# Performance work log

Hardware: AMD Instinct MI355X
Metric: run time of the kernel (lower is better)

Reference implementation:

```python
import jax, jax.numpy as jnp
import numpy as np

B, L, D, OUT, EXP = 4, 4096, 128, 55, 2
D2 = 2 * D

def _ln(x, g, b):
    m = jnp.mean(x, axis=-1, keepdims=True)
    v = jnp.mean((x - m) ** 2, axis=-1, keepdims=True)
    return (x - m) / jnp.sqrt(v + 1e-5) * g + b

def setup_inputs() -> dict:
    key = jax.random.key(0)
    ks = iter(jax.random.split(key, 32))
    w = lambda shape: jax.random.normal(next(ks), shape, jnp.float32) * 0.02
    inp = {
        'x1': jax.random.normal(next(ks), (B, L, D), jnp.float32),
        'x2': jax.random.normal(next(ks), (B, L, D), jnp.float32),
        'ln1_g': jnp.ones((D,)), 'ln1_b': jnp.zeros((D,)),
        'ln2_g': jnp.ones((D,)), 'ln2_b': jnp.zeros((D,)),
        'Wq': w((D, D)), 'bq': jnp.zeros((D,)),
        'Wv1': w((D, D)), 'bv1': jnp.zeros((D,)),
        'Wk': w((D, D)), 'bk': jnp.zeros((D,)),
        'Wv2': w((D, D)), 'bv2': jnp.zeros((D,)),
        'Wp1': w((D, D)), 'bp1': jnp.zeros((D,)),
        'Wp2': w((D, D)), 'bp2': jnp.zeros((D,)),
        'lnf_g': jnp.ones((D2,)), 'lnf_b': jnp.zeros((D2,)),
        'Wf1': w((D2, EXP * D2)), 'bf1': jnp.zeros((EXP * D2,)),
        'Wf2': w((EXP * D2, D2)), 'bf2': jnp.zeros((D2,)),
        'ln3_g': jnp.ones((D2,)), 'ln3_b': jnp.zeros((D2,)),
        'Wo': w((D2, OUT)), 'bo': jnp.zeros((OUT,)),
    }
    return inp

def reference(x1, x2, ln1_g, ln1_b, ln2_g, ln2_b, Wq, bq, Wv1, bv1, Wk, bk,
              Wv2, bv2, Wp1, bp1, Wp2, bp2, lnf_g, lnf_b, Wf1, bf1, Wf2, bf2,
              ln3_g, ln3_b, Wo, bo):
    res1, res2 = x1, x2
    x1n = _ln(x1, ln1_g, ln1_b)
    x2n = _ln(x2, ln2_g, ln2_b)
    q1 = x1n @ Wq + bq        # [B,L,D]
    v1 = x1n @ Wv1 + bv1
    k2 = x2n @ Wk + bk
    v2 = x2n @ Wv2 + bv2
    # faithful to torch: energy = einsum('bqd,bkd->bqk', keys2, queries1)
    energy = jnp.einsum('bqd,bkd->bqk', k2, q1)
    att = jax.nn.softmax(energy / jnp.sqrt(jnp.float32(D)), axis=-1)  # [B,L,L]
    out1 = jnp.einsum('bal,blv->bav', att, v1) @ Wp1 + bp1
    out2 = jnp.einsum('bal,blv->bav', att, v2) @ Wp2 + bp2
    y1 = out1 + res1
    y2 = out2 + res2
    x = jnp.concatenate([y1, y2], axis=-1)  # [B,L,2D]
    res = x
    h = _ln(x, lnf_g, lnf_b)
    h = jax.nn.gelu(h @ Wf1 + bf1, approximate=False) @ Wf2 + bf2
    x = _ln(h + res, ln3_g, ln3_b)
    return x @ Wo + bo  # [B,L,OUT]
```

## Files before the change

kernel.cpp:

```cpp
#include <hip/hip_runtime.h>
#include <hip/hip_fp16.h>

typedef _Float16 half8 __attribute__((ext_vector_type(8)));
typedef float f32x4 __attribute__((ext_vector_type(4)));
typedef long lng2 __attribute__((ext_vector_type(2)));

#define B_   4
#define L_   4096
#define D_   128
#define M_   (B_*L_)
#define D2_  256
#define H_   512
#define OUT_ 55

__device__ __forceinline__ f32x4 mfma16(half8 a, half8 b, f32x4 c) {
    return __builtin_amdgcn_mfma_f32_16x16x32_f16(a, b, c, 0, 0, 0);
}
__device__ __forceinline__ f32x4 mfma8(long a, long b, f32x4 c) {
    return __builtin_amdgcn_mfma_f32_16x16x32_fp8_fp8(a, b, c, 0, 0, 0);
}
__device__ __forceinline__ int pk4(float a, float b, float c, float d) {
    int t = __builtin_amdgcn_cvt_pk_fp8_f32(a, b, 0, false);
    return __builtin_amdgcn_cvt_pk_fp8_f32(c, d, t, true);
}
__device__ __forceinline__ float fexp2(float x) { return __builtin_amdgcn_exp2f(x); }

#define KSCL (0.08838834764831845f * 1.4426950408889634f)

#define WQ_OFF   0
#define WV1_OFF  16384
#define WK_OFF   32768
#define WV2_OFF  49152
#define WP1_OFF  65536
#define WP2_OFF  81920
#define WF1_OFF  98304
#define WF2_OFF  229376
#define WO_OFF   360448


__global__ void prep_kernel(const float* Wq, const float* Wv1, const float* Wk,
                            const float* Wv2, const float* Wp1, const float* Wp2,
                            const float* Wf1, const float* Wf2, const float* Wo,
                            _Float16* wsw, float* rowsum) {
    int id = blockIdx.y;
    int t  = blockIdx.x * 256 + threadIdx.x;
    if (id == 9) {
        if (t < 4096) ((f32x4*)rowsum)[t] = f32x4{0.f, 0.f, 0.f, 0.f};
        return;
    }
    const float* src = nullptr; int K = 0, N = 0, Npad = 0, off = 0;
    switch (id) {
        case 0: src = Wq;  K = 128; N = 128; Npad = 128; off = WQ_OFF;  break;
        case 1: src = Wv1; K = 128; N = 128; Npad = 128; off = WV1_OFF; break;
        case 2: src = Wk;  K = 128; N = 128; Npad = 128; off = WK_OFF;  break;
        case 3: src = Wv2; K = 128; N = 128; Npad = 128; off = WV2_OFF; break;
        case 4: src = Wp1; K = 128; N = 128; Npad = 128; off = WP1_OFF; break;
        case 5: src = Wp2; K = 128; N = 128; Npad = 128; off = WP2_OFF; break;
        case 6: src = Wf1; K = 256; N = 512; Npad = 512; off = WF1_OFF; break;
        case 7: src = Wf2; K = 512; N = 256; Npad = 256; off = WF2_OFF; break;
        case 8: src = Wo;  K = 256; N = 55;  Npad = 64;  off = WO_OFF;  break;
        default: return;
    }
    int total = K * Npad;
    if (t >= total) return;
    int k = t / Npad, n = t % Npad;
    float v = (n < N) ? src[k * N + n] : 0.f;
    int s = k >> 5, c = n >> 4, ln = n & 15;
    int q, j;
    if (id == 4 || id == 5) { q = (k >> 2) & 3; j = (k & 3) + (((k >> 4) & 1) << 2); }
    else                    { q = (k >> 3) & 3; j = k & 7; }
    int nc = Npad >> 4;
    wsw[off + ((size_t)((s * nc + c) * 64 + q * 16 + ln)) * 8 + j] = (_Float16)v;
}


__global__ __launch_bounds__(256) void proj_kernel(const float* x1, const float* x2,
        const _Float16* wsw,
        const float* ln1_g, const float* ln1_b, const float* ln2_g, const float* ln2_b,
        const float* bq, const float* bv1, const float* bk, const float* bv2,
        _Float16* q1, _Float16* k2, unsigned char* vsw8) {
    int g2 = blockIdx.y;
    const float* X  = g2 ? x2 : x1;
    const float* lg = g2 ? ln2_g : ln1_g;
    const float* lb = g2 ? ln2_b : ln1_b;
    int wave = threadIdx.x >> 6, lane = threadIdx.x & 63;
    int quad = lane >> 4, ln = lane & 15;
    int mbase = blockIdx.x * 64 + wave * 16;
    int lt = mbase >> 4;

    const float* xr = X + (size_t)(mbase + ln) * D_;
    float xv[4][8];
    float sum = 0.f, sq = 0.f;
    #pragma unroll
    for (int s = 0; s < 4; s++) {
        f32x4 v0 = *(const f32x4*)(xr + s * 32 + quad * 8);
        f32x4 v1 = *(const f32x4*)(xr + s * 32 + quad * 8 + 4);
        #pragma unroll
        for (int j = 0; j < 4; j++) {
            xv[s][j]     = v0[j];
            xv[s][j + 4] = v1[j];
            sum += v0[j] + v1[j];
            sq  += v0[j] * v0[j] + v1[j] * v1[j];
        }
    }
    sum += __shfl_xor(sum, 16); sum += __shfl_xor(sum, 32);
    sq  += __shfl_xor(sq, 16);  sq  += __shfl_xor(sq, 32);
    float mean = sum * (1.f / 128.f);
    float var  = sq * (1.f / 128.f) - mean * mean;
    float inv  = rsqrtf(var + 1e-5f);
    half8 a[4];
    #pragma unroll
    for (int s = 0; s < 4; s++) {
        f32x4 g0 = *(const f32x4*)(lg + s * 32 + quad * 8);
        f32x4 g1 = *(const f32x4*)(lg + s * 32 + quad * 8 + 4);
        f32x4 b0 = *(const f32x4*)(lb + s * 32 + quad * 8);
        f32x4 b1 = *(const f32x4*)(lb + s * 32 + quad * 8 + 4);
        #pragma unroll
        for (int j = 0; j < 4; j++) {
            a[s][j]     = (_Float16)((xv[s][j] - mean) * inv * g0[j] + b0[j]);
            a[s][j + 4] = (_Float16)((xv[s][j + 4] - mean) * inv * g1[j] + b1[j]);
        }
    }

    {
        const _Float16* Bw = wsw + (g2 ? WK_OFF : WQ_OFF);
        const float* bias = g2 ? bk : bq;
        float scl = g2 ? KSCL : 1.f;
        _Float16* out = g2 ? k2 : q1;
        f32x4 acc[8];
        #pragma unroll
        for (int c = 0; c < 8; c++) acc[c] = f32x4{0.f, 0.f, 0.f, 0.f};
        half8 Wc[4], Wn[4];
        #pragma unroll
        for (int s = 0; s < 4; s++)
            Wc[s] = *(const half8*)(Bw + ((size_t)((s * 8 + 0) * 64 + lane)) * 8);
        #pragma unroll
        for (int c = 0; c < 8; c++) {
            int cn = (c < 7) ? c + 1 : 7;
            #pragma unroll
            for (int s = 0; s < 4; s++)
                Wn[s] = *(const half8*)(Bw + ((size_t)((s * 8 + cn) * 64 + lane)) * 8);
            #pragma unroll
            for (int s = 0; s < 4; s++)
                acc[c] = mfma16(a[s], Wc[s], acc[c]);
            #pragma unroll
            for (int s = 0; s < 4; s++) Wc[s] = Wn[s];
        }
        #pragma unroll
        for (int c = 0; c < 8; c++) {
            int n = c * 16 + ln;
            float bv = bias[n];
            #pragma unroll
            for (int r = 0; r < 4; r++) {
                int s_o = c >> 1, q_o = ((c & 1) << 1) | (ln >> 3), j = ln & 7;
                out[((size_t)((lt * 4 + s_o) * 64 + q_o * 16 + (quad * 4 + r))) * 8 + j]
                    = (_Float16)((acc[c][r] + bv) * scl);
            }
        }
    }

    {
        const _Float16* Bw = wsw + (g2 ? WV2_OFF : WV1_OFF);
        const float* bias = g2 ? bv2 : bv1;
        int cbase = g2 ? 8 : 0;
        f32x4 acc[8];
        #pragma unroll
        for (int c = 0; c < 8; c++) acc[c] = f32x4{0.f, 0.f, 0.f, 0.f};
        half8 Wc[4], Wn[4];
        #pragma unroll
        for (int s = 0; s < 4; s++)
            Wc[s] = *(const half8*)(Bw + ((size_t)((s * 8 + 0) * 64 + lane)) * 8);
        #pragma unroll
        for (int c = 0; c < 8; c++) {
            int cn = (c < 7) ? c + 1 : 7;
            #pragma unroll
            for (int s = 0; s < 4; s++)
                Wn[s] = *(const half8*)(Bw + ((size_t)((s * 8 + cn) * 64 + lane)) * 8);
            #pragma unroll
            for (int s = 0; s < 4; s++)
                acc[c] = mfma16(a[s], Wc[s], acc[c]);
            #pragma unroll
            for (int s = 0; s < 4; s++) Wc[s] = Wn[s];
        }
        int b = mbase >> 12;
        int l0 = (mbase & (L_ - 1)) + quad * 4;
        int sp = l0 >> 6, tt = (l0 >> 4) & 3, q2 = (l0 >> 2) & 3;
        unsigned char* Vb = vsw8 + (size_t)b * (1u << 20);
        #pragma unroll
        for (int c = 0; c < 8; c++) {
            int n = c * 16 + ln;
            float bv = bias[n];
            int pk = pk4(acc[c][0] + bv, acc[c][1] + bv, acc[c][2] + bv, acc[c][3] + bv);
            *(int*)(Vb + (((size_t)(sp * 16 + cbase + c) * 64 + q2 * 16 + ln) * 16 + tt * 4)) = pk;
        }
    }
}

__global__ __launch_bounds__(256) void score_kernel(
        const _Float16* __restrict__ q1sw, const _Float16* __restrict__ k2sw,
        unsigned char* __restrict__ pmat8, float* __restrict__ rowsum) {
    int w = threadIdx.x >> 6, lane = threadIdx.x & 63;
    int quad = lane >> 4, ln = lane & 15;
    int b = blockIdx.z;
    int kL0 = blockIdx.y * 128 + (w & 1) * 64;
    int mL0 = blockIdx.x * 128 + (w >> 1) * 64;
    int ltk = ((b << 12) + kL0) >> 4;
    int ltm = ((b << 12) + mL0) >> 4;

    f32x4 acc[4][4];
    #pragma unroll
    for (int i = 0; i < 4; i++)
        #pragma unroll
        for (int j = 0; j < 4; j++) acc[i][j] = f32x4{0.f, 0.f, 0.f, 0.f};

    #pragma unroll
    for (int s = 0; s < 4; s++) {
        half8 a[4], bq[4];
        #pragma unroll
        for (int i = 0; i < 4; i++)
            a[i] = *(const half8*)(q1sw + ((size_t)(((ltk + i) * 4 + s) * 64 + lane)) * 8);
        #pragma unroll
        for (int j = 0; j < 4; j++)
            bq[j] = *(const half8*)(k2sw + ((size_t)(((ltm + j) * 4 + s) * 64 + lane)) * 8);
        #pragma unroll
        for (int i = 0; i < 4; i++)
            #pragma unroll
            for (int j = 0; j < 4; j++)
                acc[i][j] = mfma16(a[i], bq[j], acc[i][j]);
    }

    unsigned char* Pb = pmat8 + (size_t)b * (16u << 20);
    int sp = kL0 >> 6;
    #pragma unroll
    for (int j = 0; j < 4; j++) {
        int4 d;
        float csum = 0.f;
        #pragma unroll
        for (int i = 0; i < 4; i++) {
            float p0 = fexp2(acc[i][j][0]);
            float p1 = fexp2(acc[i][j][1]);
            float p2 = fexp2(acc[i][j][2]);
            float p3 = fexp2(acc[i][j][3]);
            csum += (p0 + p1) + (p2 + p3);
            ((int*)&d)[i] = pk4(p0, p1, p2, p3);
        }
        csum += __shfl_xor(csum, 16);
        csum += __shfl_xor(csum, 32);
        if (lane < 16)
            atomicAdd(&rowsum[(b << 12) + mL0 + j * 16 + ln], csum);
        int lt = (mL0 >> 4) + j;
        *(int4*)(Pb + (((size_t)(lt * 64 + sp)) * 64 + lane) * 16) = d;
    }
}

__global__ __launch_bounds__(512) void pv_kernel(
        const unsigned char* __restrict__ pmat8, const unsigned char* __restrict__ vsw8,
        const float* __restrict__ rowsum,
        _Float16* __restrict__ att1, _Float16* __restrict__ att2) {
    __shared__ f32x4 part[4][2][4][64];
    int w = threadIdx.x >> 6, lane = threadIdx.x & 63;
    int quad = lane >> 4, ln = lane & 15;
    int wc = w & 3, kh = w >> 2;
    int rowG0 = blockIdx.x * 32;
    int b = rowG0 >> 12;
    int lt0 = (rowG0 & (L_ - 1)) >> 4;
    const unsigned char* Pb = pmat8 + (size_t)b * (16u << 20);
    const unsigned char* Vb = vsw8 + (size_t)b * (1u << 20);
    int c0 = wc * 4;
    int sp0 = kh * 32;

    f32x4 acc[4][2];
    #pragma unroll
    for (int i = 0; i < 4; i++)
        #pragma unroll
        for (int c = 0; c < 2; c++) acc[i][c] = f32x4{0.f, 0.f, 0.f, 0.f};

    lng2 Vf[2][4], Pf[2][2];
    #pragma unroll
    for (int p = 0; p < 2; p++) {
        #pragma unroll
        for (int i = 0; i < 4; i++)
            Vf[p][i] = *(const lng2*)(Vb + (((size_t)((sp0 + p) * 16 + c0 + i)) * 64 + lane) * 16);
        #pragma unroll
        for (int c = 0; c < 2; c++)
            Pf[p][c] = *(const lng2*)(Pb + (((size_t)((lt0 + c) * 64 + sp0 + p)) * 64 + lane) * 16);
    }

    #define PVSTEP(buf, ii) do {                                                     \
        int spn = sp0 + ((((ii) + 2) < 32) ? (ii) + 2 : 31);                         \
        lng2 Vn[4], Pn[2];                                                           \
        _Pragma("unroll")                                                            \
        for (int i = 0; i < 4; i++)                                                  \
            Vn[i] = *(const lng2*)(Vb + (((size_t)(spn * 16 + c0 + i)) * 64 + lane) * 16); \
        _Pragma("unroll")                                                            \
        for (int c = 0; c < 2; c++)                                                  \
            Pn[c] = *(const lng2*)(Pb + (((size_t)((lt0 + c) * 64 + spn)) * 64 + lane) * 16); \
        _Pragma("unroll")                                                            \
        for (int i = 0; i < 4; i++)                                                  \
            _Pragma("unroll")                                                        \
            for (int c = 0; c < 2; c++) {                                            \
                acc[i][c] = mfma8(Vf[buf][i].x, Pf[buf][c].x, acc[i][c]);             \
                acc[i][c] = mfma8(Vf[buf][i].y, Pf[buf][c].y, acc[i][c]);             \
            }                                                                        \
        _Pragma("unroll")                                                            \
        for (int i = 0; i < 4; i++) Vf[buf][i] = Vn[i];                              \
        _Pragma("unroll")                                                            \
        for (int c = 0; c < 2; c++) Pf[buf][c] = Pn[c];                              \
    } while (0)

    for (int ii = 0; ii < 32; ii += 2) {
        PVSTEP(0, ii);
        PVSTEP(1, ii + 1);
    }
    #undef PVSTEP

    if (kh == 1) {
        #pragma unroll
        for (int i = 0; i < 4; i++)
            #pragma unroll
            for (int c = 0; c < 2; c++)
                part[wc][c][i][lane] = acc[i][c];
    }
    __syncthreads();
    if (kh == 0) {
        #pragma unroll
        for (int i = 0; i < 4; i++)
            #pragma unroll
            for (int c = 0; c < 2; c++)
                acc[i][c] += part[wc][c][i][lane];

        _Float16* att = (wc >= 2) ? att2 : att1;
        #pragma unroll
        for (int c = 0; c < 2; c++) {
            float inv = 1.f / rowsum[rowG0 + c * 16 + ln];
            int lt = (rowG0 >> 4) + c;
            #pragma unroll
            for (int sl = 0; sl < 2; sl++) {
                half8 v;
                #pragma unroll
                for (int r = 0; r < 4; r++) {
                    v[r]     = (_Float16)(acc[2 * sl][c][r] * inv);
                    v[r + 4] = (_Float16)(acc[2 * sl + 1][c][r] * inv);
                }
                int s = (wc & 1) * 2 + sl;
                *(half8*)(att + ((size_t)((lt * 4 + s) * 64 + lane)) * 8) = v;
            }
        }
    }
}

__global__ __launch_bounds__(256) void attn_out_kernel(const _Float16* att1, const _Float16* att2,
        const _Float16* wsw, const float* bp1, const float* bp2,
        const float* x1, const float* x2, const float* lnf_g, const float* lnf_b,
        _Float16* res, _Float16* xn) {
    __shared__ float sst[2][16][2][2];
    int w = threadIdx.x >> 6, lane = threadIdx.x & 63;
    int quad = lane >> 4, ln = lane & 15;
    int rt = w & 1, st = w >> 1;
    int mbase = blockIdx.x * 32 + rt * 16;
    int lt = mbase >> 4;
    const _Float16* att = st ? att2 : att1;
    const _Float16* Wp = wsw + (st ? WP2_OFF : WP1_OFF);
    const float* bp = st ? bp2 : bp1;
    const float* xres = st ? x2 : x1;

    half8 a[4];
    #pragma unroll
    for (int s = 0; s < 4; s++)
        a[s] = *(const half8*)(att + ((size_t)((lt * 4 + s) * 64 + lane)) * 8);

    f32x4 y[8];
    #pragma unroll
    for (int c = 0; c < 8; c++) y[c] = f32x4{0,0,0,0};

    half8 Wc[4], Wn[4];
    #pragma unroll
    for (int s = 0; s < 4; s++)
        Wc[s] = *(const half8*)(Wp + ((size_t)((s * 8 + 0) * 64 + lane)) * 8);
    #pragma unroll
    for (int c = 0; c < 8; c++) {
        int cn = (c < 7) ? c + 1 : 7;
        #pragma unroll
        for (int s = 0; s < 4; s++)
            Wn[s] = *(const half8*)(Wp + ((size_t)((s * 8 + cn) * 64 + lane)) * 8);
        #pragma unroll
        for (int s = 0; s < 4; s++)
            y[c] = mfma16(a[s], Wc[s], y[c]);
        #pragma unroll
        for (int s = 0; s < 4; s++) Wc[s] = Wn[s];
    }

    float psum[4] = {0,0,0,0}, psq[4] = {0,0,0,0};
    #pragma unroll
    for (int c = 0; c < 8; c++) {
        int n = c * 16 + ln;
        float bv = bp[n];
        #pragma unroll
        for (int r = 0; r < 4; r++) {
            int m = mbase + quad * 4 + r;
            float v = y[c][r] + bv + xres[(size_t)m * D_ + n];
            y[c][r] = v; psum[r] += v; psq[r] += v * v;
        }
    }
    #pragma unroll
    for (int off = 1; off < 16; off <<= 1)
        #pragma unroll
        for (int r = 0; r < 4; r++) { psum[r] += __shfl_xor(psum[r], off); psq[r] += __shfl_xor(psq[r], off); }
    if (ln == 0)
        #pragma unroll
        for (int r = 0; r < 4; r++) {
            sst[rt][quad * 4 + r][st][0] = psum[r];
            sst[rt][quad * 4 + r][st][1] = psq[r];
        }
    __syncthreads();
    #pragma unroll
    for (int r = 0; r < 4; r++) {
        float su = sst[rt][quad * 4 + r][0][0] + sst[rt][quad * 4 + r][1][0];
        float sq = sst[rt][quad * 4 + r][0][1] + sst[rt][quad * 4 + r][1][1];
        float mean = su * (1.f / 256.f);
        float var = sq * (1.f / 256.f) - mean * mean;
        float inv = rsqrtf(var + 1e-5f);
        int m = mbase + quad * 4 + r;
        int lt_m = m >> 4;
        #pragma unroll
        for (int c = 0; c < 8; c++) {
            int colg = st * 128 + c * 16 + ln;
            res[(size_t)m * D2_ + colg] = (_Float16)y[c][r];
            float yn = (y[c][r] - mean) * inv * lnf_g[colg] + lnf_b[colg];
            int s_x = colg >> 5, q_x = (colg >> 3) & 3, j = colg & 7;
            xn[((size_t)((lt_m * 8 + s_x) * 64 + q_x * 16 + (m & 15))) * 8 + j] = (_Float16)yn;
        }
    }
}

__global__ __launch_bounds__(256) void ffn1_kernel(const _Float16* xn, const _Float16* wsw,
        const float* bf1, _Float16* h) {
    int wave = threadIdx.x >> 6, lane = threadIdx.x & 63;
    int quad = lane >> 4, ln = lane & 15;
    int mbase = blockIdx.x * 64 + wave * 16;
    int lt = mbase >> 4;
    int nt = blockIdx.y;
    const _Float16* W = wsw + WF1_OFF;

    half8 a[8];
    #pragma unroll
    for (int s = 0; s < 8; s++)
        a[s] = *(const half8*)(xn + ((size_t)((lt * 8 + s) * 64 + lane)) * 8);

    f32x4 acc[8];
    #pragma unroll
    for (int c = 0; c < 8; c++) acc[c] = f32x4{0,0,0,0};

    half8 Wc[8], Wn[8];
    #pragma unroll
    for (int s = 0; s < 8; s++)
        Wc[s] = *(const half8*)(W + ((size_t)((s * 32 + nt * 8) * 64 + lane)) * 8);
    #pragma unroll
    for (int c = 0; c < 8; c++) {
        int cn = (c < 7) ? c + 1 : 7;
        #pragma unroll
        for (int s = 0; s < 8; s++)
            Wn[s] = *(const half8*)(W + ((size_t)((s * 32 + nt * 8 + cn) * 64 + lane)) * 8);
        #pragma unroll
        for (int s = 0; s < 8; s++)
            acc[c] = mfma16(a[s], Wc[s], acc[c]);
        #pragma unroll
        for (int s = 0; s < 8; s++) Wc[s] = Wn[s];
    }
    #pragma unroll
    for (int c = 0; c < 8; c++) {
        int n = nt * 128 + c * 16 + ln;
        float bv = bf1[n];
        int s_h = n >> 5, q_h = (n >> 3) & 3, j = n & 7;
        #pragma unroll
        for (int r = 0; r < 4; r++) {
            float v = acc[c][r] + bv;
            float u = 0.7978845608f * (v + 0.044715f * v * v * v);
            float e = fexp2(-2.8853900818f * u);
            float ge = v * __builtin_amdgcn_rcpf(1.f + e);
            h[((size_t)((lt * 16 + s_h) * 64 + q_h * 16 + (quad * 4 + r))) * 8 + j] = (_Float16)ge;
        }
    }
}

__global__ __launch_bounds__(256) void ffn2_out_kernel(const _Float16* h, const _Float16* wsw,
        const float* bf2, const _Float16* res, const float* g3, const float* b3,
        const float* bo, float* out) {
    __shared__ float sst[2][16][2][2];
    __shared__ _Float16 xt[8192];
    __shared__ f32x4 pc[2][4][64];
    int w = threadIdx.x >> 6, lane = threadIdx.x & 63;
    int quad = lane >> 4, ln = lane & 15;
    int rt = w & 1, nh = w >> 1;
    int mb = blockIdx.x * 32 + rt * 16;
    int lt = mb >> 4;
    const _Float16* W = wsw + WF2_OFF;

    f32x4 acc[8];
    #pragma unroll
    for (int c = 0; c < 8; c++) acc[c] = f32x4{0,0,0,0};

    half8 aC, aN;
    half8 Wc[8], Wn[8];
    aC = *(const half8*)(h + ((size_t)((lt * 16 + 0) * 64 + lane)) * 8);
    #pragma unroll
    for (int c = 0; c < 8; c++)
        Wc[c] = *(const half8*)(W + ((size_t)((0 * 16 + nh * 8 + c) * 64 + lane)) * 8);

    #pragma unroll
    for (int s = 0; s < 16; s++) {
        int sn = (s < 15) ? s + 1 : 15;
        aN = *(const half8*)(h + ((size_t)((lt * 16 + sn) * 64 + lane)) * 8);
        #pragma unroll
        for (int c = 0; c < 8; c++)
            Wn[c] = *(const half8*)(W + ((size_t)((sn * 16 + nh * 8 + c) * 64 + lane)) * 8);
        #pragma unroll
        for (int c = 0; c < 8; c++)
            acc[c] = mfma16(aC, Wc[c], acc[c]);
        aC = aN;
        #pragma unroll
        for (int c = 0; c < 8; c++) Wc[c] = Wn[c];
    }

    float y[8][4];
    float psum[4] = {0,0,0,0}, psq[4] = {0,0,0,0};
    #pragma unroll
    for (int c = 0; c < 8; c++) {
        int n = nh * 128 + c * 16 + ln;
        float bv = bf2[n];
        #pragma unroll
        for (int r = 0; r < 4; r++) {
            int m = mb + quad * 4 + r;
            float v = acc[c][r] + bv + (float)res[(size_t)m * D2_ + n];
            y[c][r] = v; psum[r] += v; psq[r] += v * v;
        }
    }
    #pragma unroll
    for (int off = 1; off < 16; off <<= 1)
        #pragma unroll
        for (int r = 0; r < 4; r++) { psum[r] += __shfl_xor(psum[r], off); psq[r] += __shfl_xor(psq[r], off); }
    if (ln == 0)
        #pragma unroll
        for (int r = 0; r < 4; r++) { sst[rt][quad * 4 + r][nh][0] = psum[r]; sst[rt][quad * 4 + r][nh][1] = psq[r]; }
    __syncthreads();
    #pragma unroll
    for (int r = 0; r < 4; r++) {
        float su = sst[rt][quad * 4 + r][0][0] + sst[rt][quad * 4 + r][1][0];
        float sq = sst[rt][quad * 4 + r][0][1] + sst[rt][quad * 4 + r][1][1];
        float mean = su * (1.f / 256.f);
        float var = sq * (1.f / 256.f) - mean * mean;
        float invs = rsqrtf(var + 1e-5f);
        #pragma unroll
        for (int c = 0; c < 8; c++) {
            int n = nh * 128 + c * 16 + ln;
            float yn = (y[c][r] - mean) * invs * g3[n] + b3[n];
            int s_x = n >> 5, q_x = (n >> 3) & 3, j = n & 7;
            xt[((rt * 8 + s_x) * 64 + q_x * 16 + (quad * 4 + r)) * 8 + j] = (_Float16)yn;
        }
    }
    __syncthreads();

    int rt2 = w & 1, kh = w >> 1;
    const _Float16* Wo = wsw + WO_OFF;
    f32x4 oacc[4];
    #pragma unroll
    for (int c = 0; c < 4; c++) oacc[c] = f32x4{0,0,0,0};
    #pragma unroll
    for (int ss = 0; ss < 4; ss++) {
        int s = kh * 4 + ss;
        half8 a = *(const half8*)(xt + ((size_t)((rt2 * 8 + s) * 64 + lane)) * 8);
        #pragma unroll
        for (int c = 0; c < 4; c++)
            oacc[c] = mfma16(a, *(const half8*)(Wo + ((size_t)((s * 4 + c) * 64 + lane)) * 8), oacc[c]);
    }
    if (kh == 1)
        #pragma unroll
        for (int c = 0; c < 4; c++) pc[rt2][c][lane] = oacc[c];
    __syncthreads();
    if (kh == 0) {
        int mb2 = blockIdx.x * 32 + rt2 * 16;
        #pragma unroll
        for (int c = 0; c < 4; c++) {
            f32x4 p = pc[rt2][c][lane];
            int n = c * 16 + ln;
            if (n < OUT_) {
                float bv = bo[n];
                #pragma unroll
                for (int r = 0; r < 4; r++)
                    out[(size_t)(mb2 + quad * 4 + r) * OUT_ + n] = oacc[c][r] + p[r] + bv;
            }
        }
    }
}

extern "C" void kernel_launch(void* const* d_in, const int* in_sizes, int n_in,
                              void* d_out, int out_size, void* d_ws, size_t ws_size,
                              hipStream_t stream) {
    const float* x1    = (const float*)d_in[0];
    const float* x2    = (const float*)d_in[1];
    const float* ln1_g = (const float*)d_in[2];
    const float* ln1_b = (const float*)d_in[3];
    const float* ln2_g = (const float*)d_in[4];
    const float* ln2_b = (const float*)d_in[5];
    const float* Wq    = (const float*)d_in[6];
    const float* bq    = (const float*)d_in[7];
    const float* Wv1   = (const float*)d_in[8];
    const float* bv1   = (const float*)d_in[9];
    const float* Wk    = (const float*)d_in[10];
    const float* bk    = (const float*)d_in[11];
    const float* Wv2   = (const float*)d_in[12];
    const float* bv2   = (const float*)d_in[13];
    const float* Wp1   = (const float*)d_in[14];
    const float* bp1   = (const float*)d_in[15];
    const float* Wp2   = (const float*)d_in[16];
    const float* bp2   = (const float*)d_in[17];
    const float* lnf_g = (const float*)d_in[18];
    const float* lnf_b = (const float*)d_in[19];
    const float* Wf1   = (const float*)d_in[20];
    const float* bf1   = (const float*)d_in[21];
    const float* Wf2   = (const float*)d_in[22];
    const float* bf2   = (const float*)d_in[23];
    const float* ln3_g = (const float*)d_in[24];
    const float* ln3_b = (const float*)d_in[25];
    const float* Wo    = (const float*)d_in[26];
    const float* bo    = (const float*)d_in[27];
    float* out = (float*)d_out;

    char* ws = (char*)d_ws;
    const size_t MB = 1 << 20;
    _Float16* q1sw   = (_Float16*)(ws + 0 * MB);
    _Float16* k2sw   = (_Float16*)(ws + 4 * MB);
    unsigned char* vsw8 = (unsigned char*)(ws + 8 * MB);
    _Float16* att1   = (_Float16*)(ws + 12 * MB);
    _Float16* att2   = (_Float16*)(ws + 16 * MB);
    _Float16* wsw    = (_Float16*)(ws + 28 * MB);
    float*    rowsum = (float*)   (ws + 29 * MB);
    _Float16* res    = (_Float16*)(ws + 30 * MB);
    _Float16* xn     = (_Float16*)(ws + 46 * MB);
    _Float16* h      = (_Float16*)(ws + 54 * MB);
    unsigned char* pmat8 = (unsigned char*)(ws + 78 * MB);

    prep_kernel<<<dim3(512, 10), 256, 0, stream>>>(Wq, Wv1, Wk, Wv2, Wp1, Wp2, Wf1, Wf2, Wo,
                                                   wsw, rowsum);
    proj_kernel<<<dim3(M_ / 64, 2), 256, 0, stream>>>(x1, x2, wsw,
                                                      ln1_g, ln1_b, ln2_g, ln2_b,
                                                      bq, bv1, bk, bv2,
                                                      q1sw, k2sw, vsw8);
    score_kernel<<<dim3(32, 32, 4), 256, 0, stream>>>(q1sw, k2sw, pmat8, rowsum);
    pv_kernel<<<dim3(M_ / 32), 512, 0, stream>>>(pmat8, vsw8, rowsum, att1, att2);
    attn_out_kernel<<<dim3(M_ / 32), 256, 0, stream>>>(att1, att2, wsw, bp1, bp2,
                                                       x1, x2, lnf_g, lnf_b, res, xn);
    ffn1_kernel<<<dim3(M_ / 64, 4), 256, 0, stream>>>(xn, wsw, bf1, h);
    ffn2_out_kernel<<<dim3(M_ / 32), 256, 0, stream>>>(h, wsw, bf2, res, ln3_g, ln3_b, bo, out);
}
```

Before: 234.1 us.

## Switch PV product to 32x32x64 scaled FP8 MFMA with new P/V layouts

Replaces the 16x16x32 fp8 MFMA in the P·V kernel with the gfx950 scaled 32x32x64 f8f6f4 MFMA, using unit scales. The score and V-projection kernels now write P and V in a swizzled layout that lets each lane load 32 contiguous bytes per operand. The intent is fewer MFMA instructions and wider, more efficient loads in the dominant PV stage. The risk is that the epilogue and write layouts must match the new accumulator lane mapping exactly, and the larger per-lane loads raise register pressure.

Result: no change. 236.0 us (+0.8%).

```diff
diff --git a/kernel.cpp b/kernel.cpp
--- a/kernel.cpp
+++ b/kernel.cpp
@@ -2,7 +2,10 @@
 #include <hip/hip_fp16.h>
 
 typedef _Float16 half8 __attribute__((ext_vector_type(8)));
+typedef _Float16 half4 __attribute__((ext_vector_type(4)));
 typedef float f32x4 __attribute__((ext_vector_type(4)));
+typedef float f32x16 __attribute__((ext_vector_type(16)));
+typedef int  i32x8 __attribute__((ext_vector_type(8)));
 typedef long lng2 __attribute__((ext_vector_type(2)));
 
 #define B_   4
@@ -16,8 +19,8 @@
 __device__ __forceinline__ f32x4 mfma16(half8 a, half8 b, f32x4 c) {
     return __builtin_amdgcn_mfma_f32_16x16x32_f16(a, b, c, 0, 0, 0);
 }
-__device__ __forceinline__ f32x4 mfma8(long a, long b, f32x4 c) {
-    return __builtin_amdgcn_mfma_f32_16x16x32_fp8_fp8(a, b, c, 0, 0, 0);
+__device__ __forceinline__ f32x16 mfma_mx32(i32x8 a, i32x8 b, f32x16 c) {
+    return __builtin_amdgcn_mfma_scale_f32_32x32x64_f8f6f4(a, b, c, 0, 0, 0, 127, 0, 127);
 }
 __device__ __forceinline__ int pk4(float a, float b, float c, float d) {
     int t = __builtin_amdgcn_cvt_pk_fp8_f32(a, b, 0, false);
@@ -183,15 +186,17 @@
             for (int s = 0; s < 4; s++) Wc[s] = Wn[s];
         }
         int b = mbase >> 12;
-        int l0 = (mbase & (L_ - 1)) + quad * 4;
-        int sp = l0 >> 6, tt = (l0 >> 4) & 3, q2 = (l0 >> 2) & 3;
+        int k64 = (mbase & (L_ - 1)) >> 6;
+        int gg = quad >> 1, jh = quad & 1;
         unsigned char* Vb = vsw8 + (size_t)b * (1u << 20);
         #pragma unroll
         for (int c = 0; c < 8; c++) {
             int n = c * 16 + ln;
             float bv = bias[n];
             int pk = pk4(acc[c][0] + bv, acc[c][1] + bv, acc[c][2] + bv, acc[c][3] + bv);
-            *(int*)(Vb + (((size_t)(sp * 16 + cbase + c) * 64 + q2 * 16 + ln) * 16 + tt * 4)) = pk;
+            int v32 = (cbase + c) >> 1;
+            int lane32 = ((c & 1) << 4) + ln + 32 * gg;
+            *(int*)(Vb + ((size_t)((k64 * 8 + v32) * 64 + lane32)) * 32 + 16 * jh + 4 * wave) = pk;
         }
     }
 }
@@ -230,7 +235,8 @@
     }
 
     unsigned char* Pb = pmat8 + (size_t)b * (16u << 20);
-    int sp = kL0 >> 6;
+    int k64 = kL0 >> 6;
+    int gg = quad >> 1, jh = quad & 1;
     #pragma unroll
     for (int j = 0; j < 4; j++) {
         int4 d;
@@ -248,8 +254,9 @@
         csum += __shfl_xor(csum, 32);
         if (lane < 16)
             atomicAdd(&rowsum[(b << 12) + mL0 + j * 16 + ln], csum);
-        int lt = (mL0 >> 4) + j;
-        *(int4*)(Pb + (((size_t)(lt * 64 + sp)) * 64 + lane) * 16) = d;
+        int att32 = (mL0 >> 5) + (j >> 1);
+        int a32 = ((j & 1) << 4) + ln;
+        *(int4*)(Pb + ((size_t)((att32 * 64 + k64) * 64 + a32 + 32 * gg)) * 32 + 16 * jh) = d;
     }
 }
 
@@ -259,91 +266,74 @@
         _Float16* __restrict__ att1, _Float16* __restrict__ att2) {
     __shared__ f32x4 part[4][2][4][64];
     int w = threadIdx.x >> 6, lane = threadIdx.x & 63;
-    int quad = lane >> 4, ln = lane & 15;
     int wc = w & 3, kh = w >> 2;
     int rowG0 = blockIdx.x * 32;
     int b = rowG0 >> 12;
-    int lt0 = (rowG0 & (L_ - 1)) >> 4;
+    int att32 = (rowG0 & (L_ - 1)) >> 5;
     const unsigned char* Pb = pmat8 + (size_t)b * (16u << 20);
     const unsigned char* Vb = vsw8 + (size_t)b * (1u << 20);
-    int c0 = wc * 4;
+
+    const unsigned char* Vbase = Vb + (size_t)(wc * 2) * 2048 + (size_t)lane * 32;
+    const unsigned char* Pbase = Pb + (size_t)att32 * 131072 + (size_t)lane * 32;
     int sp0 = kh * 32;
 
-    f32x4 acc[4][2];
-    #pragma unroll
-    for (int i = 0; i < 4; i++)
-        #pragma unroll
-        for (int c = 0; c < 2; c++) acc[i][c] = f32x4{0.f, 0.f, 0.f, 0.f};
-
-    lng2 Vf[2][4], Pf[2][2];
-    #pragma unroll
-    for (int p = 0; p < 2; p++) {
-        #pragma unroll
-        for (int i = 0; i < 4; i++)
-            Vf[p][i] = *(const lng2*)(Vb + (((size_t)((sp0 + p) * 16 + c0 + i)) * 64 + lane) * 16);
-        #pragma unroll
-        for (int c = 0; c < 2; c++)
-            Pf[p][c] = *(const lng2*)(Pb + (((size_t)((lt0 + c) * 64 + sp0 + p)) * 64 + lane) * 16);
-    }
-
-    #define PVSTEP(buf, ii) do {                                                     \
-        int spn = sp0 + ((((ii) + 2) < 32) ? (ii) + 2 : 31);                         \
-        lng2 Vn[4], Pn[2];                                                           \
-        _Pragma("unroll")                                                            \
-        for (int i = 0; i < 4; i++)                                                  \
-            Vn[i] = *(const lng2*)(Vb + (((size_t)(spn * 16 + c0 + i)) * 64 + lane) * 16); \
-        _Pragma("unroll")                                                            \
-        for (int c = 0; c < 2; c++)                                                  \
-            Pn[c] = *(const lng2*)(Pb + (((size_t)((lt0 + c) * 64 + spn)) * 64 + lane) * 16); \
-        _Pragma("unroll")                                                            \
-        for (int i = 0; i < 4; i++)                                                  \
-            _Pragma("unroll")                                                        \
-            for (int c = 0; c < 2; c++) {                                            \
-                acc[i][c] = mfma8(Vf[buf][i].x, Pf[buf][c].x, acc[i][c]);             \
-                acc[i][c] = mfma8(Vf[buf][i].y, Pf[buf][c].y, acc[i][c]);             \
-            }                                                                        \
-        _Pragma("unroll")                                                            \
-        for (int i = 0; i < 4; i++) Vf[buf][i] = Vn[i];                              \
-        _Pragma("unroll")                                                            \
-        for (int c = 0; c < 2; c++) Pf[buf][c] = Pn[c];                              \
+    f32x16 acc0, acc1;
+    #pragma unroll
+    for (int i = 0; i < 16; i++) { acc0[i] = 0.f; acc1[i] = 0.f; }
+
+    #define PVLOAD(dA, dB, dP, sp) do {                                       \
+        dA = *(const i32x8*)(Vbase + (size_t)(sp) * 16384);                   \
+        dB = *(const i32x8*)(Vbase + (size_t)(sp) * 16384 + 2048);            \
+        dP = *(const i32x8*)(Pbase + (size_t)(sp) * 2048);                    \
     } while (0)
 
+    i32x8 a0, b0, p0, a1, b1, p1, na, nb, np;
+    PVLOAD(a0, b0, p0, sp0);
+    PVLOAD(a1, b1, p1, sp0 + 1);
     for (int ii = 0; ii < 32; ii += 2) {
-        PVSTEP(0, ii);
-        PVSTEP(1, ii + 1);
-    }
-    #undef PVSTEP
+        int s2 = sp0 + ((ii + 2 < 32) ? ii + 2 : 31);
+        int s3 = sp0 + ((ii + 3 < 32) ? ii + 3 : 31);
+        PVLOAD(na, nb, np, s2);
+        acc0 = mfma_mx32(a0, p0, acc0);
+        acc1 = mfma_mx32(b0, p0, acc1);
+        a0 = na; b0 = nb; p0 = np;
+        PVLOAD(na, nb, np, s3);
+        acc0 = mfma_mx32(a1, p1, acc0);
+        acc1 = mfma_mx32(b1, p1, acc1);
+        a1 = na; b1 = nb; p1 = np;
+    }
+    #undef PVLOAD
 
     if (kh == 1) {
         #pragma unroll
-        for (int i = 0; i < 4; i++)
-            #pragma unroll
-            for (int c = 0; c < 2; c++)
-                part[wc][c][i][lane] = acc[i][c];
+        for (int q = 0; q < 4; q++) {
+            part[wc][0][q][lane] = f32x4{acc0[q * 4 + 0], acc0[q * 4 + 1],
+                                         acc0[q * 4 + 2], acc0[q * 4 + 3]};
+            part[wc][1][q][lane] = f32x4{acc1[q * 4 + 0], acc1[q * 4 + 1],
+                                         acc1[q * 4 + 2], acc1[q * 4 + 3]};
+        }
     }
     __syncthreads();
     if (kh == 0) {
-        #pragma unroll
-        for (int i = 0; i < 4; i++)
-            #pragma unroll
-            for (int c = 0; c < 2; c++)
-                acc[i][c] += part[wc][c][i][lane];
-
-        _Float16* att = (wc >= 2) ? att2 : att1;
-        #pragma unroll
-        for (int c = 0; c < 2; c++) {
-            float inv = 1.f / rowsum[rowG0 + c * 16 + ln];
-            int lt = (rowG0 >> 4) + c;
-            #pragma unroll
-            for (int sl = 0; sl < 2; sl++) {
-                half8 v;
+        int aglob = rowG0 + (lane & 31);
+        float inv = 1.f / rowsum[aglob];
+        int g = lane >> 5;
+        int lt = aglob >> 4, lnr = lane & 15;
+        #pragma unroll
+        for (int t = 0; t < 2; t++) {
+            int v32 = wc * 2 + t;
+            _Float16* att = (v32 >= 4) ? att2 : att1;
+            int s = v32 & 3;
+            #pragma unroll
+            for (int q = 0; q < 4; q++) {
+                f32x4 pp = part[wc][t][q][lane];
+                half4 hv;
                 #pragma unroll
-                for (int r = 0; r < 4; r++) {
-                    v[r]     = (_Float16)(acc[2 * sl][c][r] * inv);
-                    v[r + 4] = (_Float16)(acc[2 * sl + 1][c][r] * inv);
+                for (int rr = 0; rr < 4; rr++) {
+                    float v = ((t == 0) ? acc0[q * 4 + rr] : acc1[q * 4 + rr]) + pp[rr];
+                    hv[rr] = (_Float16)(v * inv);
                 }
-                int s = (wc & 1) * 2 + sl;
-                *(half8*)(att + ((size_t)((lt * 4 + s) * 64 + lane)) * 8) = v;
+                *(half4*)(att + ((size_t)((lt * 4 + s) * 64 + q * 16 + lnr)) * 8 + 4 * g) = hv;
             }
         }
     }
```
